# Performance work log

Hardware: AMD Instinct MI355X
Metric: run time of the kernel (lower is better)

The kernel has to match this reference:

```python
import jax, jax.numpy as jnp
import numpy as np

N_NODES = 100000
N_FEAT = 256
N_HIDDEN = 64
N_EDGES = 1600000
NEG_SLOPE = 0.05


def setup_inputs() -> dict:
    key = jax.random.key(0)
    k1, k2, k3, k4, k5 = jax.random.split(key, 5)
    x = jax.random.normal(k1, (N_NODES, N_FEAT), dtype=jnp.float32)
    W_fc = jax.random.normal(k2, (N_FEAT, N_HIDDEN), dtype=jnp.float32) * (1.0 / np.sqrt(N_FEAT))
    a_w = jax.random.normal(k3, (2 * N_HIDDEN,), dtype=jnp.float32) * (1.0 / np.sqrt(2 * N_HIDDEN))
    a_b = jax.random.normal(k4, (1,), dtype=jnp.float32) * 0.01
    edge_index = jax.random.randint(k5, (2, N_EDGES), 0, N_NODES, dtype=jnp.int64)
    return {"x": x, "W_fc": W_fc, "a_w": a_w, "a_b": a_b, "edge_index": edge_index}


def reference(x, W_fc, a_w, a_b, edge_index):
    n = x.shape[0]
    src = edge_index[0]  # row indices i
    dst = edge_index[1]  # col indices j
    Wh = x @ W_fc                                  # [N, H]
    Wh_i = Wh[src]                                  # [E, H] gather
    Wh_j = Wh[dst]                                  # [E, H] gather
    # a([Wh_i, Wh_j]) == Wh_i @ a_w[:H] + Wh_j @ a_w[H:] + a_b  (avoids materializing concat)
    H = Wh.shape[1]
    score = Wh_i @ a_w[:H] + Wh_j @ a_w[H:] + a_b[0]  # [E]
    h = jnp.exp(jax.nn.leaky_relu(score, negative_slope=NEG_SLOPE))  # [E]
    h_sum = jax.ops.segment_sum(h, src, num_segments=n)              # scatter_add over source nodes
    alpha = h / h_sum[src]                                           # edge-softmax weights
    # sparse.mm(adj_att, Wh): out[i] = sum_{(i,j) in E} alpha_ij * Wh[j]
    out = jax.ops.segment_sum(alpha[:, None] * Wh_j, src, num_segments=n)  # [N, H]
    return (out, alpha)
```

## Files before the change

### kernel.cpp

```cpp
#include <hip/hip_runtime.h>

#define N_NODES 100000
#define N_FEAT  256
#define N_HID   64
#define N_EDGES 1600000
#define NEG_SLOPE 0.05f

#define NBUCKET 391
#define TILE    2048
#define NTILES  ((N_EDGES + TILE - 1) / TILE)
#define BCAP    4704
#define BTHREADS 1024

typedef float  floatx4 __attribute__((ext_vector_type(4)));
typedef short  shortx8 __attribute__((ext_vector_type(8)));

__device__ __forceinline__ unsigned short f2bf(float f) {
  unsigned int u = __float_as_uint(f);
  u = u + 0x7fffu + ((u >> 16) & 1u);
  return (unsigned short)(u >> 16);
}
__device__ __forceinline__ float bf_lo(unsigned int u) {
  return __uint_as_float(u << 16);
}
__device__ __forceinline__ float bf_hi(unsigned int u) {
  return __uint_as_float(u & 0xFFFF0000u);
}

__device__ __forceinline__ int wave_iscan(int v, int lane) {
#pragma unroll
  for (int d = 1; d < 64; d <<= 1) {
    int tv = __shfl_up(v, d);
    if (lane >= d) v += tv;
  }
  return v;
}

__global__ __launch_bounds__(256) void k_wprep(const float* __restrict__ W,
                                               unsigned short* __restrict__ WbT) {
  int n = blockIdx.x;
  int k = threadIdx.x;
  WbT[n * 256 + k] = f2bf(W[(size_t)k * N_HID + n]);
}

#define WSTRIDE 264
__global__ __launch_bounds__(256) void k_gemm(
    const float* __restrict__ x, const unsigned short* __restrict__ WbT,
    const float* __restrict__ aw, unsigned short* __restrict__ Whb,
    float* __restrict__ s1, float* __restrict__ s2) {
  __shared__ unsigned short wsm[64 * WSTRIDE];

  const int t = threadIdx.x;
  for (int idx = t; idx < 64 * 32; idx += 256) {
    int row = idx >> 5, c16 = idx & 31;
    *(uint4*)(wsm + row * WSTRIDE + c16 * 8) =
        *(const uint4*)(WbT + row * 256 + c16 * 8);
  }
  __syncthreads();

  const int w = t >> 6;
  const int lane = t & 63;
  const int q = lane >> 4;
  const int li = lane & 15;
  const int r0 = blockIdx.x * 64;
  const int grow = r0 + w * 16 + li;
  const bool vrow = grow < N_NODES;

  float4 araw[16];
  if (vrow) {
    const float4* xr = (const float4*)(x + (size_t)grow * N_FEAT);
#pragma unroll
    for (int c = 0; c < 8; ++c) {
      araw[2 * c]     = xr[c * 8 + q * 2];
      araw[2 * c + 1] = xr[c * 8 + q * 2 + 1];
    }
  } else {
#pragma unroll
    for (int i = 0; i < 16; ++i) araw[i] = make_float4(0.f, 0.f, 0.f, 0.f);
  }

  floatx4 acc[4];
#pragma unroll
  for (int g = 0; g < 4; ++g) acc[g] = (floatx4){0.f, 0.f, 0.f, 0.f};

#pragma unroll
  for (int c = 0; c < 8; ++c) {
    float4 v0 = araw[2 * c], v1 = araw[2 * c + 1];
    shortx8 a;
    a[0] = (short)f2bf(v0.x); a[1] = (short)f2bf(v0.y);
    a[2] = (short)f2bf(v0.z); a[3] = (short)f2bf(v0.w);
    a[4] = (short)f2bf(v1.x); a[5] = (short)f2bf(v1.y);
    a[6] = (short)f2bf(v1.z); a[7] = (short)f2bf(v1.w);
#pragma unroll
    for (int g = 0; g < 4; ++g) {
      shortx8 b = *(const shortx8*)(wsm + (g * 16 + li) * WSTRIDE + c * 32 + q * 8);
      acc[g] = __builtin_amdgcn_mfma_f32_16x16x32_bf16(a, b, acc[g], 0, 0, 0);
    }
  }

#pragma unroll
  for (int j = 0; j < 4; ++j) {
    int r = r0 + w * 16 + q * 4 + j;
    if (r < N_NODES) {
#pragma unroll
      for (int g = 0; g < 4; ++g)
        Whb[(size_t)r * N_HID + g * 16 + li] = f2bf(acc[g][j]);
    }
  }

#pragma unroll
  for (int j = 0; j < 4; ++j) {
    float p1 = 0.f, p2 = 0.f;
#pragma unroll
    for (int g = 0; g < 4; ++g) {
      p1 += acc[g][j] * aw[g * 16 + li];
      p2 += acc[g][j] * aw[64 + g * 16 + li];
    }
#pragma unroll
    for (int off = 1; off < 16; off <<= 1) {
      p1 += __shfl_xor(p1, off);
      p2 += __shfl_xor(p2, off);
    }
    int r = r0 + w * 16 + q * 4 + j;
    if (li == 0 && r < N_NODES) {
      s1[r] = p1;
      s2[r] = p2;
    }
  }
}

__global__ __launch_bounds__(256) void k_histT(const int* __restrict__ ei,
                                               int* __restrict__ tileCnt) {
  __shared__ int hist[NBUCKET];
  const int t = threadIdx.x;
  const int e0 = blockIdx.x * TILE;
  const int ecnt = min(TILE, N_EDGES - e0);

  for (int i = t; i < NBUCKET; i += 256) hist[i] = 0;
  __syncthreads();

#pragma unroll
  for (int j = 0; j < 8; ++j) {
    int li = j * 256 + t;
    if (li < ecnt) atomicAdd(&hist[ei[e0 + li] >> 8], 1);
  }
  __syncthreads();

  for (int b = t; b < NBUCKET; b += 256)
    tileCnt[blockIdx.x * NBUCKET + b] = hist[b];
}

__global__ __launch_bounds__(1024) void k_tilescan(
    const int* __restrict__ tileCnt, int* __restrict__ tileOff,
    int* __restrict__ buckTot) {
  __shared__ int wtot[16];
  const int b = blockIdx.x;
  const int t = threadIdx.x;
  const int lane = t & 63, wv = t >> 6;
  int v = (t < NTILES) ? tileCnt[t * NBUCKET + b] : 0;
  int p = wave_iscan(v, lane);
  if (lane == 63) wtot[wv] = p;
  __syncthreads();
  int off = 0;
  for (int w2 = 0; w2 < wv; ++w2) off += wtot[w2];
  if (t < NTILES) tileOff[t * NBUCKET + b] = off + p - v;
  if (t == 0) {
    int tot = 0;
#pragma unroll
    for (int w2 = 0; w2 < 16; ++w2) tot += wtot[w2];
    buckTot[b] = tot;
  }
}

__global__ __launch_bounds__(512) void k_bstart(const int* __restrict__ buckTot,
                                                int* __restrict__ buckStart) {
  __shared__ int wtot[8];
  const int t = threadIdx.x;
  const int lane = t & 63, wv = t >> 6;
  int v = (t < NBUCKET) ? buckTot[t] : 0;
  int p = wave_iscan(v, lane);
  if (lane == 63) wtot[wv] = p;
  __syncthreads();
  int off = 0;
  for (int w2 = 0; w2 < wv; ++w2) off += wtot[w2];
  if (t < NBUCKET) buckStart[t] = off + p - v;
  if (t == 0) buckStart[NBUCKET] = N_EDGES;
}

__global__ __launch_bounds__(256) void k_bin(
    const int* __restrict__ ei, const float* __restrict__ s1,
    const float* __restrict__ s2, const float* __restrict__ ab,
    const int* __restrict__ tileCnt, const int* __restrict__ tileOff,
    const int* __restrict__ buckStart, int2* __restrict__ binned,
    float* __restrict__ h_orig) {
  __shared__ int  hist[NBUCKET];
  __shared__ int  scanx[NBUCKET];
  __shared__ int  fillc[NBUCKET];
  __shared__ int  gbase[NBUCKET];
  __shared__ int  wtot[4];
  __shared__ int2 sorted[TILE];
  __shared__ int  tgt[TILE];

  const int t = threadIdx.x;
  const int tile = blockIdx.x;
  const int e0 = tile * TILE;
  const int ecnt = min(TILE, N_EDGES - e0);
  const int lane = t & 63, wv = t >> 6;

  for (int b = t; b < NBUCKET; b += 256) {
    hist[b] = tileCnt[tile * NBUCKET + b];
    gbase[b] = buckStart[b] + tileOff[tile * NBUCKET + b];
    fillc[b] = 0;
  }
  __syncthreads();

  int b0 = t * 2, b1 = t * 2 + 1;
  int v0 = (b0 < NBUCKET) ? hist[b0] : 0;
  int v1 = (b1 < NBUCKET) ? hist[b1] : 0;
  int pairsum = v0 + v1;
  int p = wave_iscan(pairsum, lane);
  if (lane == 63) wtot[wv] = p;
  __syncthreads();
  int off = 0;
  for (int w2 = 0; w2 < wv; ++w2) off += wtot[w2];
  int base = off + p - pairsum;
  if (b0 < NBUCKET) scanx[b0] = base;
  if (b1 < NBUCKET) scanx[b1] = base + v0;
  __syncthreads();

  float bias = ab[0];
#pragma unroll
  for (int j = 0; j < 8; ++j) {
    int li = j * 256 + t;
    if (li < ecnt) {
      int idx = e0 + li;
      int src = ei[idx];
      int dst = ei[N_EDGES + idx];
      float sc = s1[src] + s2[dst] + bias;
      float v = sc > 0.f ? sc : NEG_SLOPE * sc;
      float h = __expf(v);
      h_orig[idx] = h;
      int b = src >> 8;
      int slot = scanx[b] + atomicAdd(&fillc[b], 1);
      sorted[slot].x = dst | ((src & 255) << 17);
      sorted[slot].y = __float_as_int(h);
      tgt[slot] = gbase[b] + (slot - scanx[b]);
    }
  }
  __syncthreads();

  for (int i = t; i < ecnt; i += 256) binned[tgt[i]] = sorted[i];
}

__global__ __launch_bounds__(BTHREADS, 8) void k_bucket(
    const int* __restrict__ buckStart, const int2* __restrict__ binned,
    const unsigned short* __restrict__ Whb, float* __restrict__ out,
    float* __restrict__ invh) {
  __shared__ int2  recs[BCAP];
  __shared__ int   startp[256];
  __shared__ int   curs[256];
  __shared__ int   wtot[4];

  const int t = threadIdx.x;
  const int lane = t & 63, wvx = t >> 6;
  const int b = blockIdx.x;
  const int node0 = b * 256;
  const int W0 = buckStart[b];
  const int W1 = buckStart[b + 1];
  const int cnt = W1 - W0;

  if (t < 256) curs[t] = 0;
  __syncthreads();

  for (int i = t; i < cnt; i += BTHREADS) {
    int rx = binned[W0 + i].x;
    atomicAdd(&curs[(rx >> 17) & 255], 1);
  }
  __syncthreads();

  int v = 0;
  if (t < 256) v = curs[t];
  int p = wave_iscan(v, lane);
  if (t < 256 && lane == 63) wtot[wvx] = p;
  __syncthreads();
  if (t < 256) {
    int off = 0;
    for (int w2 = 0; w2 < wvx; ++w2) off += wtot[w2];
    int mystart = off + p - v;
    startp[t] = mystart;
    curs[t] = mystart;
  }
  __syncthreads();

  for (int i = t; i < cnt; i += BTHREADS) {
    int2 r = binned[W0 + i];
    int loc = (r.x >> 17) & 255;
    int slot = atomicAdd(&curs[loc], 1);
    if (slot < BCAP) {
      recs[slot].x = r.x & 0x1FFFF;
      recs[slot].y = r.y;
    }
  }
  __syncthreads();

  const int wv = t >> 6, lane2 = t & 63;
  const int grp = (wv << 3) | (lane2 >> 3);
  const int li = lane2 & 7;
  for (int j = grp; j < 256; j += 128) {
    int n2 = node0 + j;
    if (n2 >= N_NODES) break;
    int beg = startp[j];
    int endp = curs[j];
    if (endp > BCAP) endp = BCAP;
    float hs = 0.f;
    float acc[8] = {};
    int r = beg;
    for (; r + 4 <= endp; r += 4) {
      int2 e0 = recs[r];
      int2 e1 = recs[r + 1];
      int2 e2 = recs[r + 2];
      int2 e3 = recs[r + 3];
      uint4 w0 = *(const uint4*)(Whb + (size_t)e0.x * N_HID + li * 8);
      uint4 w1 = *(const uint4*)(Whb + (size_t)e1.x * N_HID + li * 8);
      uint4 w2 = *(const uint4*)(Whb + (size_t)e2.x * N_HID + li * 8);
      uint4 w3 = *(const uint4*)(Whb + (size_t)e3.x * N_HID + li * 8);
      float a0 = __int_as_float(e0.y);
      float a1 = __int_as_float(e1.y);
      float a2 = __int_as_float(e2.y);
      float a3 = __int_as_float(e3.y);
      hs += (a0 + a1) + (a2 + a3);
      acc[0] += a0 * bf_lo(w0.x); acc[1] += a0 * bf_hi(w0.x);
      acc[2] += a0 * bf_lo(w0.y); acc[3] += a0 * bf_hi(w0.y);
      acc[4] += a0 * bf_lo(w0.z); acc[5] += a0 * bf_hi(w0.z);
      acc[6] += a0 * bf_lo(w0.w); acc[7] += a0 * bf_hi(w0.w);
      acc[0] += a1 * bf_lo(w1.x); acc[1] += a1 * bf_hi(w1.x);
      acc[2] += a1 * bf_lo(w1.y); acc[3] += a1 * bf_hi(w1.y);
      acc[4] += a1 * bf_lo(w1.z); acc[5] += a1 * bf_hi(w1.z);
      acc[6] += a1 * bf_lo(w1.w); acc[7] += a1 * bf_hi(w1.w);
      acc[0] += a2 * bf_lo(w2.x); acc[1] += a2 * bf_hi(w2.x);
      acc[2] += a2 * bf_lo(w2.y); acc[3] += a2 * bf_hi(w2.y);
      acc[4] += a2 * bf_lo(w2.z); acc[5] += a2 * bf_hi(w2.z);
      acc[6] += a2 * bf_lo(w2.w); acc[7] += a2 * bf_hi(w2.w);
      acc[0] += a3 * bf_lo(w3.x); acc[1] += a3 * bf_hi(w3.x);
      acc[2] += a3 * bf_lo(w3.y); acc[3] += a3 * bf_hi(w3.y);
      acc[4] += a3 * bf_lo(w3.z); acc[5] += a3 * bf_hi(w3.z);
      acc[6] += a3 * bf_lo(w3.w); acc[7] += a3 * bf_hi(w3.w);
    }
    for (; r < endp; ++r) {
      int2 rec = recs[r];
      float a = __int_as_float(rec.y);
      hs += a;
      uint4 wvv = *(const uint4*)(Whb + (size_t)rec.x * N_HID + li * 8);
      acc[0] += a * bf_lo(wvv.x); acc[1] += a * bf_hi(wvv.x);
      acc[2] += a * bf_lo(wvv.y); acc[3] += a * bf_hi(wvv.y);
      acc[4] += a * bf_lo(wvv.z); acc[5] += a * bf_hi(wvv.z);
      acc[6] += a * bf_lo(wvv.w); acc[7] += a * bf_hi(wvv.w);
    }
    float inv = (endp > beg) ? 1.f / hs : 0.f;
    if (li == 0) invh[n2] = inv;
#pragma unroll
    for (int k = 0; k < 8; ++k) acc[k] *= inv;
    float* op = out + (size_t)n2 * N_HID + li * 8;
    *(float4*)op = make_float4(acc[0], acc[1], acc[2], acc[3]);
    *(float4*)(op + 4) = make_float4(acc[4], acc[5], acc[6], acc[7]);
  }
}

__global__ __launch_bounds__(256) void k_alpha(
    const int* __restrict__ ei, const float* __restrict__ h_orig,
    const float* __restrict__ invh, float* __restrict__ alpha) {
  int e = blockIdx.x * 256 + threadIdx.x;
  if (e >= N_EDGES) return;
  alpha[e] = h_orig[e] * invh[ei[e]];
}

extern "C" void kernel_launch(void* const* d_in, const int* in_sizes, int n_in,
                              void* d_out, int out_size, void* d_ws,
                              size_t ws_size, hipStream_t stream) {
  const float* x  = (const float*)d_in[0];
  const float* W  = (const float*)d_in[1];
  const float* aw = (const float*)d_in[2];
  const float* ab = (const float*)d_in[3];
  const int*   ei = (const int*)d_in[4];

  float* out   = (float*)d_out;
  float* alpha = out + (size_t)N_NODES * N_HID;

  unsigned short* Whb = (unsigned short*)d_ws;
  unsigned short* WbT = Whb + (size_t)N_NODES * N_HID;
  float* s1      = (float*)(WbT + 16384);
  float* s2      = s1 + N_NODES;
  float* invh    = s2 + N_NODES;
  int2*  binned  = (int2*)(invh + N_NODES);
  float* h_orig  = (float*)(binned + N_EDGES);
  int*   tileCnt = (int*)(h_orig + N_EDGES);
  int*   tileOff = tileCnt + NTILES * NBUCKET;
  int*   buckTot = tileOff + NTILES * NBUCKET;
  int*   buckStart = buckTot + NBUCKET;

  k_wprep<<<64, 256, 0, stream>>>(W, WbT);
  k_histT<<<NTILES, 256, 0, stream>>>(ei, tileCnt);
  k_tilescan<<<NBUCKET, 1024, 0, stream>>>(tileCnt, tileOff, buckTot);
  k_bstart<<<1, 512, 0, stream>>>(buckTot, buckStart);

  k_gemm<<<(N_NODES + 63) / 64, 256, 0, stream>>>(x, WbT, aw, Whb, s1, s2);

  k_bin<<<NTILES, 256, 0, stream>>>(ei, s1, s2, ab, tileCnt, tileOff,
                                    buckStart, binned, h_orig);
  k_bucket<<<NBUCKET, BTHREADS, 0, stream>>>(buckStart, binned, Whb, out, invh);
  k_alpha<<<(N_EDGES + 255) / 256, 256, 0, stream>>>(ei, h_orig, invh, alpha);
}
```

Measured before the change: 265.6 us.

## Replace exact edge-bucket prefix scans with fixed-capacity buckets and atomic cursors

```diff
diff --git a/kernel.cpp b/kernel.cpp
--- a/kernel.cpp
+++ b/kernel.cpp
@@ -37,10 +37,13 @@
 }
 
 __global__ __launch_bounds__(256) void k_wprep(const float* __restrict__ W,
-                                               unsigned short* __restrict__ WbT) {
+                                               unsigned short* __restrict__ WbT,
+                                               int* __restrict__ cursor) {
   int n = blockIdx.x;
   int k = threadIdx.x;
   WbT[n * 256 + k] = f2bf(W[(size_t)k * N_HID + n]);
+  int i = blockIdx.x * 256 + threadIdx.x;
+  if (i < NBUCKET) cursor[i] = 0;
 }
 
 #define WSTRIDE 264
@@ -129,69 +132,10 @@
   }
 }
 
-__global__ __launch_bounds__(256) void k_histT(const int* __restrict__ ei,
-                                               int* __restrict__ tileCnt) {
-  __shared__ int hist[NBUCKET];
-  const int t = threadIdx.x;
-  const int e0 = blockIdx.x * TILE;
-  const int ecnt = min(TILE, N_EDGES - e0);
-
-  for (int i = t; i < NBUCKET; i += 256) hist[i] = 0;
-  __syncthreads();
-
-#pragma unroll
-  for (int j = 0; j < 8; ++j) {
-    int li = j * 256 + t;
-    if (li < ecnt) atomicAdd(&hist[ei[e0 + li] >> 8], 1);
-  }
-  __syncthreads();
-
-  for (int b = t; b < NBUCKET; b += 256)
-    tileCnt[blockIdx.x * NBUCKET + b] = hist[b];
-}
-
-__global__ __launch_bounds__(1024) void k_tilescan(
-    const int* __restrict__ tileCnt, int* __restrict__ tileOff,
-    int* __restrict__ buckTot) {
-  __shared__ int wtot[16];
-  const int b = blockIdx.x;
-  const int t = threadIdx.x;
-  const int lane = t & 63, wv = t >> 6;
-  int v = (t < NTILES) ? tileCnt[t * NBUCKET + b] : 0;
-  int p = wave_iscan(v, lane);
-  if (lane == 63) wtot[wv] = p;
-  __syncthreads();
-  int off = 0;
-  for (int w2 = 0; w2 < wv; ++w2) off += wtot[w2];
-  if (t < NTILES) tileOff[t * NBUCKET + b] = off + p - v;
-  if (t == 0) {
-    int tot = 0;
-#pragma unroll
-    for (int w2 = 0; w2 < 16; ++w2) tot += wtot[w2];
-    buckTot[b] = tot;
-  }
-}
-
-__global__ __launch_bounds__(512) void k_bstart(const int* __restrict__ buckTot,
-                                                int* __restrict__ buckStart) {
-  __shared__ int wtot[8];
-  const int t = threadIdx.x;
-  const int lane = t & 63, wv = t >> 6;
-  int v = (t < NBUCKET) ? buckTot[t] : 0;
-  int p = wave_iscan(v, lane);
-  if (lane == 63) wtot[wv] = p;
-  __syncthreads();
-  int off = 0;
-  for (int w2 = 0; w2 < wv; ++w2) off += wtot[w2];
-  if (t < NBUCKET) buckStart[t] = off + p - v;
-  if (t == 0) buckStart[NBUCKET] = N_EDGES;
-}
-
 __global__ __launch_bounds__(256) void k_bin(
     const int* __restrict__ ei, const float* __restrict__ s1,
     const float* __restrict__ s2, const float* __restrict__ ab,
-    const int* __restrict__ tileCnt, const int* __restrict__ tileOff,
-    const int* __restrict__ buckStart, int2* __restrict__ binned,
+    int* __restrict__ cursor, int2* __restrict__ binned,
     float* __restrict__ h_orig) {
   __shared__ int  hist[NBUCKET];
   __shared__ int  scanx[NBUCKET];
@@ -208,9 +152,15 @@
   const int lane = t & 63, wv = t >> 6;
 
   for (int b = t; b < NBUCKET; b += 256) {
-    hist[b] = tileCnt[tile * NBUCKET + b];
-    gbase[b] = buckStart[b] + tileOff[tile * NBUCKET + b];
+    hist[b] = 0;
     fillc[b] = 0;
+  }
+  __syncthreads();
+
+#pragma unroll
+  for (int j = 0; j < 8; ++j) {
+    int li = j * 256 + t;
+    if (li < ecnt) atomicAdd(&hist[ei[e0 + li] >> 8], 1);
   }
   __syncthreads();
 
@@ -224,8 +174,14 @@
   int off = 0;
   for (int w2 = 0; w2 < wv; ++w2) off += wtot[w2];
   int base = off + p - pairsum;
-  if (b0 < NBUCKET) scanx[b0] = base;
-  if (b1 < NBUCKET) scanx[b1] = base + v0;
+  if (b0 < NBUCKET) {
+    scanx[b0] = base;
+    gbase[b0] = b0 * BCAP + (v0 ? atomicAdd(&cursor[b0], v0) : 0);
+  }
+  if (b1 < NBUCKET) {
+    scanx[b1] = base + v0;
+    gbase[b1] = b1 * BCAP + (v1 ? atomicAdd(&cursor[b1], v1) : 0);
+  }
   __syncthreads();
 
   float bias = ab[0];
@@ -244,16 +200,20 @@
       int slot = scanx[b] + atomicAdd(&fillc[b], 1);
       sorted[slot].x = dst | ((src & 255) << 17);
       sorted[slot].y = __float_as_int(h);
-      tgt[slot] = gbase[b] + (slot - scanx[b]);
-    }
-  }
-  __syncthreads();
-
-  for (int i = t; i < ecnt; i += 256) binned[tgt[i]] = sorted[i];
+      int g = gbase[b] + (slot - scanx[b]);
+      tgt[slot] = (g < (b + 1) * BCAP) ? g : -1;
+    }
+  }
+  __syncthreads();
+
+  for (int i = t; i < ecnt; i += 256) {
+    int g = tgt[i];
+    if (g >= 0) binned[g] = sorted[i];
+  }
 }
 
 __global__ __launch_bounds__(BTHREADS, 8) void k_bucket(
-    const int* __restrict__ buckStart, const int2* __restrict__ binned,
+    const int* __restrict__ cursor, const int2* __restrict__ binned,
     const unsigned short* __restrict__ Whb, float* __restrict__ out,
     float* __restrict__ invh) {
   __shared__ int2  recs[BCAP];
@@ -265,9 +225,8 @@
   const int lane = t & 63, wvx = t >> 6;
   const int b = blockIdx.x;
   const int node0 = b * 256;
-  const int W0 = buckStart[b];
-  const int W1 = buckStart[b + 1];
-  const int cnt = W1 - W0;
+  const int W0 = b * BCAP;
+  const int cnt = min(cursor[b], BCAP);
 
   if (t < 256) curs[t] = 0;
   __syncthreads();
@@ -392,21 +351,12 @@
   float* s2      = s1 + N_NODES;
   float* invh    = s2 + N_NODES;
   int2*  binned  = (int2*)(invh + N_NODES);
-  float* h_orig  = (float*)(binned + N_EDGES);
-  int*   tileCnt = (int*)(h_orig + N_EDGES);
-  int*   tileOff = tileCnt + NTILES * NBUCKET;
-  int*   buckTot = tileOff + NTILES * NBUCKET;
-  int*   buckStart = buckTot + NBUCKET;
-
-  k_wprep<<<64, 256, 0, stream>>>(W, WbT);
-  k_histT<<<NTILES, 256, 0, stream>>>(ei, tileCnt);
-  k_tilescan<<<NBUCKET, 1024, 0, stream>>>(tileCnt, tileOff, buckTot);
-  k_bstart<<<1, 512, 0, stream>>>(buckTot, buckStart);
-
+  float* h_orig  = (float*)(binned + (size_t)NBUCKET * BCAP);
+  int*   cursor  = (int*)(h_orig + N_EDGES);
+
+  k_wprep<<<64, 256, 0, stream>>>(W, WbT, cursor);
   k_gemm<<<(N_NODES + 63) / 64, 256, 0, stream>>>(x, WbT, aw, Whb, s1, s2);
-
-  k_bin<<<NTILES, 256, 0, stream>>>(ei, s1, s2, ab, tileCnt, tileOff,
-                                    buckStart, binned, h_orig);
-  k_bucket<<<NBUCKET, BTHREADS, 0, stream>>>(buckStart, binned, Whb, out, invh);
+  k_bin<<<NTILES, 256, 0, stream>>>(ei, s1, s2, ab, cursor, binned, h_orig);
+  k_bucket<<<NBUCKET, BTHREADS, 0, stream>>>(cursor, binned, Whb, out, invh);
   k_alpha<<<(N_EDGES + 255) / 256, 256, 0, stream>>>(ei, h_orig, invh, alpha);
 }
```

Result: slower. 279.8 us (+5.3%).
